# Kernel tuning notes

Hardware: AMD Instinct MI355X
Metric: run time of the kernel (lower is better)

## Reference

```python
import jax, jax.numpy as jnp
import numpy as np

N_NODES = 100000
N_EDGES = 1600000


def spmm(rows, cols, vals, z):
    # out[i] = sum_{e: rows[e]==i} vals[e] * z[cols[e]]  (COO sparse-dense matmul)
    msgs = vals[:, None] * z[cols]  # [E, d] gather + scale
    return jax.ops.segment_sum(msgs, rows, num_segments=N_NODES)


def setup_inputs() -> dict:
    key = jax.random.key(0)
    k1, k2, k3, k4, k5, k6, k7, k8 = jax.random.split(key, 8)
    rows = jax.random.randint(k1, (N_EDGES,), 0, N_NODES, dtype=jnp.int32)
    cols = jax.random.randint(k2, (N_EDGES,), 0, N_NODES, dtype=jnp.int32)
    vals = jax.random.uniform(k3, (N_EDGES,), dtype=jnp.float32)
    x = jax.random.normal(k4, (N_NODES, 128), dtype=jnp.float32)
    # Linear layers per n_feats = [128, 128, 64]; stored as [in, out] (z @ W + b)
    W1 = jax.random.normal(k5, (128, 128), dtype=jnp.float32) * (1.0 / np.sqrt(128))
    b1 = jax.random.normal(k6, (128,), dtype=jnp.float32) * 0.01
    W2 = jax.random.normal(k7, (128, 64), dtype=jnp.float32) * (1.0 / np.sqrt(128))
    b2 = jax.random.normal(k8, (64,), dtype=jnp.float32) * 0.01
    return {"rows": rows, "cols": cols, "vals": vals, "x": x,
            "W1": W1, "b1": b1, "W2": W2, "b2": b2}


def reference(rows, cols, vals, x, W1, b1, W2, b2):
    # layer 1: activation(spmm(a, linear(x)))
    z = jax.nn.relu(spmm(rows, cols, vals, x @ W1 + b1))
    # last layer: spmm(a, linear(z)) with no activation
    z = spmm(rows, cols, vals, z @ W2 + b2)
    return z
```

## Files before the change

kernel.cpp:

```cpp
#include <hip/hip_runtime.h>

typedef unsigned int uint;
typedef unsigned short ushort;
typedef unsigned long long u64;
typedef float f32x4 __attribute__((ext_vector_type(4)));

#define NN 100000
#define NE 1600000
#define NBUCK ((NN + 255) >> 8)

__device__ __forceinline__ ushort f2bf(float f) {
    uint u = __float_as_uint(f);
    u += 0x7FFFu + ((u >> 16) & 1u);
    return (ushort)(u >> 16);
}
__device__ __forceinline__ float bf2f(ushort h) {
    return __uint_as_float(((uint)h) << 16);
}

template <typename TIN, int M, int ROWS>
__global__ __launch_bounds__(256) void gemm_kernel(
    const TIN* __restrict__ X, const float* __restrict__ W,
    const float* __restrict__ b, ushort* __restrict__ Y, int N)
{
    constexpr int K  = 128;
    constexpr int CG = M / 4;
    constexpr int RG = 256 / CG;
    constexpr int RPT = ROWS / RG;
    static_assert(RPT == 4, "expect 4 rows per thread");

    __shared__ float xt[K * ROWS];
    __shared__ float Ws[64 * M];

    const int tid  = threadIdx.x;
    const int row0 = blockIdx.x * ROWS;

    for (int i = tid; i < ROWS * (K / 4); i += 256) {
        int r  = i % ROWS;
        int k4 = i / ROWS;
        int rr = row0 + r;
        if (rr >= N) rr = N - 1;
        float v0, v1, v2, v3;
        if constexpr (sizeof(TIN) == 4) {
            f32x4 v = __builtin_nontemporal_load(
                reinterpret_cast<const f32x4*>(X) + rr * (K / 4) + k4);
            v0 = v.x; v1 = v.y; v2 = v.z; v3 = v.w;
        } else {
            ushort4 v = reinterpret_cast<const ushort4*>(X)[rr * (K / 4) + k4];
            v0 = bf2f(v.x); v1 = bf2f(v.y); v2 = bf2f(v.z); v3 = bf2f(v.w);
        }
        xt[(k4 * 4 + 0) * ROWS + r] = v0;
        xt[(k4 * 4 + 1) * ROWS + r] = v1;
        xt[(k4 * 4 + 2) * ROWS + r] = v2;
        xt[(k4 * 4 + 3) * ROWS + r] = v3;
    }

    const int cg = tid % CG;
    const int rg = tid / CG;
    const int c0 = cg * 4;
    const int r0 = rg * RPT;

    float acc[4][4];
    {
        float4 bv = reinterpret_cast<const float4*>(b)[cg];
        #pragma unroll
        for (int i = 0; i < 4; ++i) {
            acc[i][0] = bv.x; acc[i][1] = bv.y; acc[i][2] = bv.z; acc[i][3] = bv.w;
        }
    }

    for (int kh = 0; kh < 2; ++kh) {
        __syncthreads();
        for (int i = tid; i < 64 * (M / 4); i += 256) {
            reinterpret_cast<float4*>(Ws)[i] =
                reinterpret_cast<const float4*>(W)[kh * 64 * (M / 4) + i];
        }
        __syncthreads();

        #pragma unroll 4
        for (int kk = 0; kk < 64; ++kk) {
            const int k = kh * 64 + kk;
            float4 xv = *reinterpret_cast<const float4*>(&xt[k * ROWS + r0]);
            float4 wv = *reinterpret_cast<const float4*>(&Ws[kk * M + c0]);
            acc[0][0] += xv.x * wv.x; acc[0][1] += xv.x * wv.y;
            acc[0][2] += xv.x * wv.z; acc[0][3] += xv.x * wv.w;
            acc[1][0] += xv.y * wv.x; acc[1][1] += xv.y * wv.y;
            acc[1][2] += xv.y * wv.z; acc[1][3] += xv.y * wv.w;
            acc[2][0] += xv.z * wv.x; acc[2][1] += xv.z * wv.y;
            acc[2][2] += xv.z * wv.z; acc[2][3] += xv.z * wv.w;
            acc[3][0] += xv.w * wv.x; acc[3][1] += xv.w * wv.y;
            acc[3][2] += xv.w * wv.z; acc[3][3] += xv.w * wv.w;
        }
    }

    #pragma unroll
    for (int i = 0; i < 4; ++i) {
        int rr = row0 + r0 + i;
        if (rr < N) {
            u64 o = (u64)f2bf(acc[i][0])
                  | ((u64)f2bf(acc[i][1]) << 16)
                  | ((u64)f2bf(acc[i][2]) << 32)
                  | ((u64)f2bf(acc[i][3]) << 48);
            *reinterpret_cast<u64*>(&Y[rr * M + c0]) = o;
        }
    }
}

__global__ __launch_bounds__(256) void bucket_hist_kernel(
    const int* __restrict__ rows, int* __restrict__ gcnt)
{
    __shared__ int cnt[NBUCK];
    const int tid = threadIdx.x;
    for (int i = tid; i < NBUCK; i += 256) cnt[i] = 0;
    __syncthreads();
    #pragma unroll
    for (int q = 0; q < 4; ++q) {
        int vi = blockIdx.x * 1024 + q * 256 + tid;
        if (vi < NE / 4) {
            int4 r = reinterpret_cast<const int4*>(rows)[vi];
            atomicAdd(&cnt[r.x >> 8], 1); atomicAdd(&cnt[r.y >> 8], 1);
            atomicAdd(&cnt[r.z >> 8], 1); atomicAdd(&cnt[r.w >> 8], 1);
        }
    }
    __syncthreads();
    for (int i = tid; i < NBUCK; i += 256)
        if (cnt[i]) atomicAdd(&gcnt[i], cnt[i]);
}

__global__ __launch_bounds__(512) void scan_kernel(
    const int* __restrict__ gcnt, int* __restrict__ bstart, int* __restrict__ gfill)
{
    __shared__ int s[512];
    const int tid = threadIdx.x;
    int v = (tid < NBUCK) ? gcnt[tid] : 0;
    s[tid] = v;
    __syncthreads();
    for (int off = 1; off < 512; off <<= 1) {
        int t = (tid >= off) ? s[tid - off] : 0;
        __syncthreads();
        s[tid] += t;
        __syncthreads();
    }
    if (tid < NBUCK) {
        bstart[tid] = s[tid] - v;
        gfill[tid]  = s[tid] - v;
    }
    if (tid == 0) bstart[NBUCK] = NE;
}

__global__ __launch_bounds__(1024) void bin_kernel(
    const int* __restrict__ rows, const int* __restrict__ cols,
    const float* __restrict__ vals, int* __restrict__ gfill,
    u64* __restrict__ es_stage)
{
    __shared__ int cnt[NBUCK];
    __shared__ int base[NBUCK];
    const int tid = threadIdx.x;

    for (int i = tid; i < NBUCK; i += 1024) cnt[i] = 0;
    __syncthreads();

    int r[8];
    #pragma unroll
    for (int q = 0; q < 8; ++q) {
        int e = blockIdx.x * 8192 + q * 1024 + tid;
        r[q] = (e < NE) ? rows[e] : -1;
        if (r[q] >= 0) atomicAdd(&cnt[r[q] >> 8], 1);
    }
    __syncthreads();

    for (int i = tid; i < NBUCK; i += 1024)
        base[i] = cnt[i] ? atomicAdd(&gfill[i], cnt[i]) : 0;
    __syncthreads();
    for (int i = tid; i < NBUCK; i += 1024) cnt[i] = 0;
    __syncthreads();

    #pragma unroll
    for (int q = 0; q < 8; ++q) {
        if (r[q] >= 0) {
            int e = blockIdx.x * 8192 + q * 1024 + tid;
            int bk = r[q] >> 8;
            int pos = base[bk] + atomicAdd(&cnt[bk], 1);
            uint lo = (uint)(r[q] & 255) | ((uint)cols[e] << 8);
            es_stage[pos] = (u64)lo | ((u64)(uint)__float_as_uint(vals[e]) << 32);
        }
    }
}

__global__ __launch_bounds__(1024) void finalize_kernel(
    const int* __restrict__ bstart, const u64* __restrict__ es_stage,
    int* __restrict__ row_ptr, u64* __restrict__ es)
{
    __shared__ int cnt[256];
    __shared__ int scn[256];
    __shared__ int fill[256];
    const int b    = blockIdx.x;
    const int tid  = threadIdx.x;
    const int row0 = b << 8;
    const int s = bstart[b];
    const int e = bstart[b + 1];

    if (tid < 256) cnt[tid] = 0;
    __syncthreads();

    for (int i = s + tid; i < e; i += 1024)
        atomicAdd(&cnt[(uint)es_stage[i] & 255u], 1);
    __syncthreads();

    if (tid < 256) scn[tid] = cnt[tid];
    __syncthreads();
    for (int off = 1; off < 256; off <<= 1) {
        int t = (tid < 256 && tid >= off) ? scn[tid - off] : 0;
        __syncthreads();
        if (tid < 256) scn[tid] += t;
        __syncthreads();
    }
    if (tid < 256) {
        int start = s + scn[tid] - cnt[tid];
        fill[tid] = start;
        int rr = row0 + tid;
        if (rr <= NN) row_ptr[rr] = start;
    }
    __syncthreads();

    for (int i = s + tid; i < e; i += 1024) {
        u64 pk = es_stage[i];
        uint lo = (uint)pk;
        int pos = atomicAdd(&fill[lo & 255u], 1);
        es[pos] = (pk & 0xFFFFFFFF00000000ull) | (u64)(lo >> 8);
    }
}

template <int D, bool BF16_RELU_OUT>
__global__ __launch_bounds__(256) void spmm_gather(
    const int* __restrict__ row_ptr, const u64* __restrict__ es,
    const ushort* __restrict__ Zb, void* __restrict__ outv)
{
    const int row  = (blockIdx.x * 256 + threadIdx.x) >> 6;
    const int lane = threadIdx.x & 63;
    if (row >= NN) return;
    const int start = row_ptr[row];
    const int end   = row_ptr[row + 1];

    float accx = 0.f, accy = 0.f;

    for (int base = start; base < end; base += 64) {
        const int m = min(end - base, 64);
        int c = 0, vb = 0;
        if (lane < m) {
            u64 e = es[base + lane];
            c  = (int)(uint)(e & 0xFFFFFFFFu);
            vb = (int)(uint)(e >> 32);
        }

        int j = 0;
        for (; j + 8 <= m; j += 8) {
            int cc[8]; float vv[8];
            #pragma unroll
            for (int q = 0; q < 8; ++q) {
                cc[q] = __shfl(c, j + q);
                vv[q] = __int_as_float(__shfl(vb, j + q));
            }
            if (D == 128) {
                uint z[8];
                #pragma unroll
                for (int q = 0; q < 8; ++q)
                    z[q] = *reinterpret_cast<const uint*>(&Zb[(size_t)cc[q] * 128 + 2 * lane]);
                #pragma unroll
                for (int q = 0; q < 8; ++q) {
                    accx += vv[q] * __uint_as_float(z[q] << 16);
                    accy += vv[q] * __uint_as_float(z[q] & 0xFFFF0000u);
                }
            } else {
                float z[8];
                #pragma unroll
                for (int q = 0; q < 8; ++q)
                    z[q] = bf2f(Zb[(size_t)cc[q] * 64 + lane]);
                #pragma unroll
                for (int q = 0; q < 8; ++q)
                    accx += vv[q] * z[q];
            }
        }
        for (; j < m; ++j) {
            int   cj = __shfl(c, j);
            float vj = __int_as_float(__shfl(vb, j));
            if (D == 128) {
                uint z = *reinterpret_cast<const uint*>(&Zb[(size_t)cj * 128 + 2 * lane]);
                accx += vj * __uint_as_float(z << 16);
                accy += vj * __uint_as_float(z & 0xFFFF0000u);
            } else {
                accx += vj * bf2f(Zb[(size_t)cj * 64 + lane]);
            }
        }
    }

    if (BF16_RELU_OUT) {
        uint o = (uint)f2bf(fmaxf(accx, 0.f)) | ((uint)f2bf(fmaxf(accy, 0.f)) << 16);
        reinterpret_cast<uint*>(outv)[(size_t)row * 64 + lane] = o;
    } else if (D == 128) {
        float2 o = make_float2(accx, accy);
        *reinterpret_cast<float2*>(&reinterpret_cast<float*>(outv)[(size_t)row * 128 + 2 * lane]) = o;
    } else {
        __builtin_nontemporal_store(accx, &reinterpret_cast<float*>(outv)[(size_t)row * 64 + lane]);
    }
}

extern "C" void kernel_launch(void* const* d_in, const int* in_sizes, int n_in,
                              void* d_out, int out_size, void* d_ws, size_t ws_size,
                              hipStream_t stream)
{
    const int*   rows = (const int*)  d_in[0];
    const int*   cols = (const int*)  d_in[1];
    const float* vals = (const float*)d_in[2];
    const float* x    = (const float*)d_in[3];
    const float* W1   = (const float*)d_in[4];
    const float* b1   = (const float*)d_in[5];
    const float* W2   = (const float*)d_in[6];
    const float* b2   = (const float*)d_in[7];
    float* out = (float*)d_out;

    char* ws = (char*)d_ws;
    size_t off = 0;
    ushort* h1b    = (ushort*)(ws + off); off += (size_t)NN * 128 * sizeof(ushort);
    ushort* s1b    = (ushort*)(ws + off); off += (size_t)NN * 128 * sizeof(ushort);
    ushort* h2b    = (ushort*)(ws + off); off += (size_t)NN * 64 * sizeof(ushort);
    u64*    es     = (u64*)   (ws + off); off += (size_t)NE * sizeof(u64);
    int*    row_ptr= (int*)   (ws + off); off += (size_t)(NN + 1) * sizeof(int);
    int*    gcnt   = (int*)   (ws + off); off += (size_t)NBUCK * sizeof(int);
    int*    bstart = (int*)   (ws + off); off += (size_t)(NBUCK + 1) * sizeof(int);
    int*    gfill  = (int*)   (ws + off); off += (size_t)NBUCK * sizeof(int);
    u64*    es_stage = (u64*)h1b;

    hipMemsetAsync(gcnt, 0, (size_t)NBUCK * sizeof(int), stream);
    bucket_hist_kernel<<<(NE / 4 + 1023) / 1024, 256, 0, stream>>>(rows, gcnt);
    scan_kernel<<<1, 512, 0, stream>>>(gcnt, bstart, gfill);
    bin_kernel<<<(NE + 8191) / 8192, 1024, 0, stream>>>(rows, cols, vals, gfill, es_stage);
    finalize_kernel<<<NBUCK, 1024, 0, stream>>>(bstart, es_stage, row_ptr, es);

    gemm_kernel<float, 128, 32><<<NN / 32, 256, 0, stream>>>(x, W1, b1, h1b, NN);
    spmm_gather<128, true><<<(NN * 64 + 255) / 256, 256, 0, stream>>>(row_ptr, es, h1b, s1b);

    gemm_kernel<ushort, 64, 64><<<(NN + 63) / 64, 256, 0, stream>>>(s1b, W2, b2, h2b, NN);
    spmm_gather<64, false><<<(NN * 64 + 255) / 256, 256, 0, stream>>>(row_ptr, es, h2b, out);
}
```

Before: 364.7 us.

## Replace FP32 FMA GEMMs with bf16 MFMA kernels using pre-transposed weights

Replaces the scalar FP32 register-tiled GEMMs with a kernel that uses 16x16x32 bf16 MFMA instructions. Each wave computes a 16-row slice of a 64-row tile. A small prep kernel converts W1 and W2 to bf16 and transposes them so B fragments can be loaded contiguously from padded LDS. Inputs are converted to bf16 in LDS, and outputs are staged through LDS so global stores are coalesced. Rounding x and the weights to bf16 lowers precision. The change also adds one extra small kernel launch.

```diff
diff --git a/kernel.cpp b/kernel.cpp
--- a/kernel.cpp
+++ b/kernel.cpp
@@ -4,6 +4,7 @@
 typedef unsigned short ushort;
 typedef unsigned long long u64;
 typedef float f32x4 __attribute__((ext_vector_type(4)));
+typedef short bf16x8 __attribute__((ext_vector_type(8)));
 
 #define NN 100000
 #define NE 1600000
@@ -18,90 +19,102 @@
     return __uint_as_float(((uint)h) << 16);
 }
 
-template <typename TIN, int M, int ROWS>
-__global__ __launch_bounds__(256) void gemm_kernel(
-    const TIN* __restrict__ X, const float* __restrict__ W,
+__global__ __launch_bounds__(256) void prep_w_kernel(
+    const float* __restrict__ W1, const float* __restrict__ W2,
+    ushort* __restrict__ Wt1, ushort* __restrict__ Wt2)
+{
+    int t = blockIdx.x * 256 + threadIdx.x;
+    if (t < 128 * 128) {
+        int c = t & 127, k = t >> 7;
+        Wt1[c * 128 + k] = f2bf(W1[k * 128 + c]);
+    }
+    if (t < 64 * 128) {
+        int c = t & 63, k = t >> 6;
+        Wt2[c * 128 + k] = f2bf(W2[k * 64 + c]);
+    }
+}
+
+template <typename TIN, int M>
+__global__ __launch_bounds__(256) void gemm_mfma(
+    const TIN* __restrict__ X, const ushort* __restrict__ Wt,
     const float* __restrict__ b, ushort* __restrict__ Y, int N)
 {
-    constexpr int K  = 128;
-    constexpr int CG = M / 4;
-    constexpr int RG = 256 / CG;
-    constexpr int RPT = ROWS / RG;
-    static_assert(RPT == 4, "expect 4 rows per thread");
-
-    __shared__ float xt[K * ROWS];
-    __shared__ float Ws[64 * M];
+    constexpr int NT = M / 16;
+    constexpr int PITCH = 136;
+    __shared__ ushort xt[64 * PITCH];
+    __shared__ ushort wt[M * PITCH];
 
     const int tid  = threadIdx.x;
-    const int row0 = blockIdx.x * ROWS;
-
-    for (int i = tid; i < ROWS * (K / 4); i += 256) {
-        int r  = i % ROWS;
-        int k4 = i / ROWS;
+    const int row0 = blockIdx.x * 64;
+
+    for (int i = tid; i < M * 32; i += 256) {
+        int c = i >> 5, kc = i & 31;
+        u64 w4 = reinterpret_cast<const u64*>(Wt)[c * 32 + kc];
+        *reinterpret_cast<u64*>(&wt[c * PITCH + kc * 4]) = w4;
+    }
+    for (int i = tid; i < 64 * 32; i += 256) {
+        int r = i >> 5, kc = i & 31;
         int rr = row0 + r;
         if (rr >= N) rr = N - 1;
-        float v0, v1, v2, v3;
+        ushort4 o;
         if constexpr (sizeof(TIN) == 4) {
             f32x4 v = __builtin_nontemporal_load(
-                reinterpret_cast<const f32x4*>(X) + rr * (K / 4) + k4);
-            v0 = v.x; v1 = v.y; v2 = v.z; v3 = v.w;
+                reinterpret_cast<const f32x4*>(X) + (size_t)rr * 32 + kc);
+            o.x = f2bf(v.x); o.y = f2bf(v.y); o.z = f2bf(v.z); o.w = f2bf(v.w);
         } else {
-            ushort4 v = reinterpret_cast<const ushort4*>(X)[rr * (K / 4) + k4];
-            v0 = bf2f(v.x); v1 = bf2f(v.y); v2 = bf2f(v.z); v3 = bf2f(v.w);
-        }
-        xt[(k4 * 4 + 0) * ROWS + r] = v0;
-        xt[(k4 * 4 + 1) * ROWS + r] = v1;
-        xt[(k4 * 4 + 2) * ROWS + r] = v2;
-        xt[(k4 * 4 + 3) * ROWS + r] = v3;
-    }
-
-    const int cg = tid % CG;
-    const int rg = tid / CG;
-    const int c0 = cg * 4;
-    const int r0 = rg * RPT;
-
-    float acc[4][4];
-    {
-        float4 bv = reinterpret_cast<const float4*>(b)[cg];
+            u64 v = reinterpret_cast<const u64*>(X)[(size_t)rr * 32 + kc];
+            o.x = (ushort)v; o.y = (ushort)(v >> 16);
+            o.z = (ushort)(v >> 32); o.w = (ushort)(v >> 48);
+        }
+        *reinterpret_cast<u64*>(&xt[r * PITCH + kc * 4]) =
+            (u64)o.x | ((u64)o.y << 16) | ((u64)o.z << 32) | ((u64)o.w << 48);
+    }
+    __syncthreads();
+
+    const int wave = tid >> 6, lane = tid & 63;
+    const int lrow = lane & 15;
+    const int kgrp = lane >> 4;
+
+    bf16x8 a[4];
+    #pragma unroll
+    for (int ks = 0; ks < 4; ++ks)
+        a[ks] = *reinterpret_cast<bf16x8*>(
+            &xt[(wave * 16 + lrow) * PITCH + ks * 32 + kgrp * 8]);
+
+    f32x4 acc[NT];
+    #pragma unroll
+    for (int nt = 0; nt < NT; ++nt) {
+        float bv = b[nt * 16 + lrow];
+        acc[nt].x = bv; acc[nt].y = bv; acc[nt].z = bv; acc[nt].w = bv;
+    }
+
+    #pragma unroll
+    for (int nt = 0; nt < NT; ++nt) {
         #pragma unroll
-        for (int i = 0; i < 4; ++i) {
-            acc[i][0] = bv.x; acc[i][1] = bv.y; acc[i][2] = bv.z; acc[i][3] = bv.w;
-        }
-    }
-
-    for (int kh = 0; kh < 2; ++kh) {
-        __syncthreads();
-        for (int i = tid; i < 64 * (M / 4); i += 256) {
-            reinterpret_cast<float4*>(Ws)[i] =
-                reinterpret_cast<const float4*>(W)[kh * 64 * (M / 4) + i];
-        }
-        __syncthreads();
-
-        #pragma unroll 4
-        for (int kk = 0; kk < 64; ++kk) {
-            const int k = kh * 64 + kk;
-            float4 xv = *reinterpret_cast<const float4*>(&xt[k * ROWS + r0]);
-            float4 wv = *reinterpret_cast<const float4*>(&Ws[kk * M + c0]);
-            acc[0][0] += xv.x * wv.x; acc[0][1] += xv.x * wv.y;
-            acc[0][2] += xv.x * wv.z; acc[0][3] += xv.x * wv.w;
-            acc[1][0] += xv.y * wv.x; acc[1][1] += xv.y * wv.y;
-            acc[1][2] += xv.y * wv.z; acc[1][3] += xv.y * wv.w;
-            acc[2][0] += xv.z * wv.x; acc[2][1] += xv.z * wv.y;
-            acc[2][2] += xv.z * wv.z; acc[2][3] += xv.z * wv.w;
-            acc[3][0] += xv.w * wv.x; acc[3][1] += xv.w * wv.y;
-            acc[3][2] += xv.w * wv.z; acc[3][3] += xv.w * wv.w;
-        }
-    }
-
-    #pragma unroll
-    for (int i = 0; i < 4; ++i) {
-        int rr = row0 + r0 + i;
+        for (int ks = 0; ks < 4; ++ks) {
+            bf16x8 bf = *reinterpret_cast<bf16x8*>(
+                &wt[(nt * 16 + lrow) * PITCH + ks * 32 + kgrp * 8]);
+            acc[nt] = __builtin_amdgcn_mfma_f32_16x16x32_bf16(a[ks], bf, acc[nt], 0, 0, 0);
+        }
+    }
+
+    __syncthreads();
+    #pragma unroll
+    for (int nt = 0; nt < NT; ++nt) {
+        #pragma unroll
+        for (int j = 0; j < 4; ++j) {
+            int rloc = wave * 16 + kgrp * 4 + j;
+            xt[rloc * PITCH + nt * 16 + lrow] = f2bf(acc[nt][j]);
+        }
+    }
+    __syncthreads();
+    for (int i = tid; i < 64 * (M / 4); i += 256) {
+        int r  = i / (M / 4);
+        int c4 = i % (M / 4);
+        int rr = row0 + r;
         if (rr < N) {
-            u64 o = (u64)f2bf(acc[i][0])
-                  | ((u64)f2bf(acc[i][1]) << 16)
-                  | ((u64)f2bf(acc[i][2]) << 32)
-                  | ((u64)f2bf(acc[i][3]) << 48);
-            *reinterpret_cast<u64*>(&Y[rr * M + c0]) = o;
+            u64 o = *reinterpret_cast<u64*>(&xt[r * PITCH + c4 * 4]);
+            *reinterpret_cast<u64*>(&Y[(size_t)rr * M + c4 * 4]) = o;
         }
     }
 }
@@ -329,17 +342,20 @@
     int*    gcnt   = (int*)   (ws + off); off += (size_t)NBUCK * sizeof(int);
     int*    bstart = (int*)   (ws + off); off += (size_t)(NBUCK + 1) * sizeof(int);
     int*    gfill  = (int*)   (ws + off); off += (size_t)NBUCK * sizeof(int);
+    ushort* Wt1    = (ushort*)(ws + off); off += (size_t)128 * 128 * sizeof(ushort);
+    ushort* Wt2    = (ushort*)(ws + off); off += (size_t)64 * 128 * sizeof(ushort);
     u64*    es_stage = (u64*)h1b;
 
     hipMemsetAsync(gcnt, 0, (size_t)NBUCK * sizeof(int), stream);
+    prep_w_kernel<<<64, 256, 0, stream>>>(W1, W2, Wt1, Wt2);
     bucket_hist_kernel<<<(NE / 4 + 1023) / 1024, 256, 0, stream>>>(rows, gcnt);
     scan_kernel<<<1, 512, 0, stream>>>(gcnt, bstart, gfill);
     bin_kernel<<<(NE + 8191) / 8192, 1024, 0, stream>>>(rows, cols, vals, gfill, es_stage);
     finalize_kernel<<<NBUCK, 1024, 0, stream>>>(bstart, es_stage, row_ptr, es);
 
-    gemm_kernel<float, 128, 32><<<NN / 32, 256, 0, stream>>>(x, W1, b1, h1b, NN);
+    gemm_mfma<float, 128><<<(NN + 63) / 64, 256, 0, stream>>>(x, Wt1, b1, h1b, NN);
     spmm_gather<128, true><<<(NN * 64 + 255) / 256, 256, 0, stream>>>(row_ptr, es, h1b, s1b);
 
-    gemm_kernel<ushort, 64, 64><<<(NN + 63) / 64, 256, 0, stream>>>(s1b, W2, b2, h2b, NN);
+    gemm_mfma<ushort, 64><<<(NN + 63) / 64, 256, 0, stream>>>(s1b, Wt2, b2, h2b, NN);
     spmm_gather<64, false><<<(NN * 64 + 255) / 256, 256, 0, stream>>>(row_ptr, es, h2b, out);
 }
```

After: 319.3 us. 1.14x faster.
